# Optimization experiments

Measured on AMD Instinct MI355X. Metric: run time of the kernel, lower is better.

Reference implementation:

```python
import jax, jax.numpy as jnp
import numpy as np

B, N, M, D = 8, 4096, 4096, 3

def setup_inputs() -> dict:
    key = jax.random.key(0)
    ks = jax.random.split(key, 6)
    return {
        "X_pred": jax.random.normal(ks[0], (B, N, D), dtype=jnp.float32),
        "X_true": jax.random.normal(ks[1], (B, M, D), dtype=jnp.float32),
        "R_pred": jax.random.normal(ks[2], (B, D, D), dtype=jnp.float32),
        "t_pred": jax.random.normal(ks[3], (B, D), dtype=jnp.float32),
        "R_true": jax.random.normal(ks[4], (B, D, D), dtype=jnp.float32),
        "t_true": jax.random.normal(ks[5], (B, D), dtype=jnp.float32),
        "temperature": jnp.asarray(0.1, dtype=jnp.float32),
    }

def reference(X_pred, X_true, R_pred, t_pred, R_true, t_true, temperature):
    # Rigid transforms: x' = R x + t
    Xp = jnp.einsum('bij,bnj->bni', R_pred, X_pred) + t_pred[:, None, :]  # (B,N,D)
    Xt = jnp.einsum('bij,bmj->bmi', R_true, X_true) + t_true[:, None, :]  # (B,M,D)
    # Squared pairwise distances: |a|^2 + |b|^2 - 2 a.b  (== cdist(p=2)**2)
    sq_p = jnp.sum(Xp * Xp, axis=-1)  # (B,N)
    sq_t = jnp.sum(Xt * Xt, axis=-1)  # (B,M)
    dist_sq = sq_p[:, :, None] + sq_t[:, None, :] - 2.0 * jnp.einsum('bnd,bmd->bnm', Xp, Xt)
    dist_sq = jnp.maximum(dist_sq, 0.0)  # (B,N,M)
    soft_alignment = jax.nn.softmax(-dist_sq / temperature, axis=-1)
    weighted_distances = jnp.sum(soft_alignment * dist_sq, axis=-1)  # (B,N)
    return jnp.mean(weighted_distances)
```

## Files before the change

kernel.cpp:

```cpp
#include <hip/hip_runtime.h>


#define B_    8
#define N_    4096
#define M_    4096
#define NWAVE 8
#define BLOCK (NWAVE * 64)
#define ROWS  256
#define MSPL  8
#define QCH   (M_ / MSPL)
#define WQ    (QCH / NWAVE)
#define LOG2E 1.4426950408889634f
#define LN2   0.6931471805599453f
#define BIGF  3.0e38f

__global__ __launch_bounds__(BLOCK, 8) void softfape_main(
    const float* __restrict__ X_pred, const float* __restrict__ X_true,
    const float* __restrict__ R_pred, const float* __restrict__ t_pred,
    const float* __restrict__ R_true, const float* __restrict__ t_true,
    const float* __restrict__ temp,
    float4* __restrict__ Pg)
{
    __shared__ float4 Q[QCH];
    __shared__ float  Mp[NWAVE][ROWS];
    __shared__ float  Lp[NWAVE][ROWS];
    __shared__ float  Sp[NWAVE][ROWS];

    const int tid  = threadIdx.x;
    const int wave = tid >> 6;
    const int lane = tid & 63;
    const int x    = blockIdx.x;
    const int ms   = x & 7;
    const int rg   = (x >> 3) & 15;
    const int b    = x >> 7;

    const float T   = temp[0];
    const float c   = LOG2E / T;
    const float m2c = -2.0f * c;

    if (tid < QCH / 2) {
        const float g00 = R_true[b*9+0], g01 = R_true[b*9+1], g02 = R_true[b*9+2];
        const float g10 = R_true[b*9+3], g11 = R_true[b*9+4], g12 = R_true[b*9+5];
        const float g20 = R_true[b*9+6], g21 = R_true[b*9+7], g22 = R_true[b*9+8];
        const float u0  = t_true[b*3+0], u1 = t_true[b*3+1], u2 = t_true[b*3+2];
        const float2* xt = (const float2*)(X_true + ((size_t)b * M_ + ms * QCH) * 3);
        const float2 f0 = xt[3*tid+0], f1 = xt[3*tid+1], f2 = xt[3*tid+2];
        {
            const float y0 = fmaf(g00, f0.x, fmaf(g01, f0.y, fmaf(g02, f1.x, u0)));
            const float y1 = fmaf(g10, f0.x, fmaf(g11, f0.y, fmaf(g12, f1.x, u1)));
            const float y2 = fmaf(g20, f0.x, fmaf(g21, f0.y, fmaf(g22, f1.x, u2)));
            const float nn = fmaf(y0, y0, fmaf(y1, y1, y2 * y2));
            Q[2*tid]   = make_float4(m2c*y0, m2c*y1, m2c*y2, c*nn);
        }
        {
            const float y0 = fmaf(g00, f1.y, fmaf(g01, f2.x, fmaf(g02, f2.y, u0)));
            const float y1 = fmaf(g10, f1.y, fmaf(g11, f2.x, fmaf(g12, f2.y, u1)));
            const float y2 = fmaf(g20, f1.y, fmaf(g21, f2.x, fmaf(g22, f2.y, u2)));
            const float nn = fmaf(y0, y0, fmaf(y1, y1, y2 * y2));
            Q[2*tid+1] = make_float4(m2c*y0, m2c*y1, m2c*y2, c*nn);
        }
    }

    float px[4], py[4], pz[4], pw[4];
    {
        const float h00 = R_pred[b*9+0], h01 = R_pred[b*9+1], h02 = R_pred[b*9+2];
        const float h10 = R_pred[b*9+3], h11 = R_pred[b*9+4], h12 = R_pred[b*9+5];
        const float h20 = R_pred[b*9+6], h21 = R_pred[b*9+7], h22 = R_pred[b*9+8];
        const float v0 = t_pred[b*3+0], v1 = t_pred[b*3+1], v2 = t_pred[b*3+2];
        const float4* xp = (const float4*)(X_pred + ((size_t)b * N_ + rg * ROWS + lane * 4) * 3);
        const float4 a0 = xp[0], a1 = xp[1], a2 = xp[2];
        const float rx[4] = {a0.x, a0.w, a1.z, a2.y};
        const float ry[4] = {a0.y, a1.x, a1.w, a2.z};
        const float rz[4] = {a0.z, a1.y, a2.x, a2.w};
        #pragma unroll
        for (int r = 0; r < 4; ++r) {
            px[r] = fmaf(h00, rx[r], fmaf(h01, ry[r], fmaf(h02, rz[r], v0)));
            py[r] = fmaf(h10, rx[r], fmaf(h11, ry[r], fmaf(h12, rz[r], v1)));
            pz[r] = fmaf(h20, rx[r], fmaf(h21, ry[r], fmaf(h22, rz[r], v2)));
            pw[r] = c * fmaf(px[r], px[r], fmaf(py[r], py[r], pz[r] * pz[r]));
        }
    }

    __syncthreads();

    float mr[4] = {BIGF, BIGF, BIGF, BIGF};
    float L[4]  = {0.f, 0.f, 0.f, 0.f};
    float S[4]  = {0.f, 0.f, 0.f, 0.f};
    const float4* __restrict__ Qw = Q + wave * WQ;
    #pragma unroll 2
    for (int k = 0; k < WQ; ++k) {
        const float4 q = Qw[k];
        #pragma unroll
        for (int r = 0; r < 4; ++r) {
            const float A  = fmaf(q.x, px[r], fmaf(q.y, py[r], fmaf(q.z, pz[r], q.w)));
            const float d  = A + pw[r];
            const float mN = fminf(mr[r], d);
            const float sc = __builtin_amdgcn_exp2f(mN - mr[r]);
            const float w  = __builtin_amdgcn_exp2f(mN - d);
            L[r] = fmaf(L[r], sc, w);
            S[r] = fmaf(S[r], sc, w * d);
            mr[r] = mN;
        }
    }

    #pragma unroll
    for (int r = 0; r < 4; ++r) {
        Mp[wave][4*lane + r] = mr[r];
        Lp[wave][4*lane + r] = L[r];
        Sp[wave][4*lane + r] = S[r];
    }
    __syncthreads();

    if (tid < ROWS) {
        float m = BIGF, Lr = 0.0f, Sr = 0.0f;
        #pragma unroll
        for (int w2 = 0; w2 < NWAVE; ++w2) {
            const float mw = Mp[w2][tid];
            const float lw = Lp[w2][tid];
            const float sw = Sp[w2][tid];
            const float mN = fminf(m, mw);
            const float e1 = __builtin_amdgcn_exp2f(mN - m);
            const float e2 = __builtin_amdgcn_exp2f(mN - mw);
            Lr = Lr * e1 + lw * e2;
            Sr = Sr * e1 + sw * e2;
            m = mN;
        }
        const size_t row = (size_t)b * N_ + rg * ROWS + tid;
        Pg[row * MSPL + ms] = make_float4(m, Lr, Sr, 0.0f);
    }
}

__global__ __launch_bounds__(256) void softfape_finalize(
    const float4* __restrict__ Pg, const float* __restrict__ temp,
    float* __restrict__ out)
{
    __shared__ float ws4[4];
    const int tid = threadIdx.x;
    const size_t row = (size_t)blockIdx.x * 256 + tid;

    float m = BIGF, L = 0.0f, S = 0.0f;
    #pragma unroll
    for (int i = 0; i < MSPL; ++i) {
        const float4 P = Pg[row * MSPL + i];
        const float mN = fminf(m, P.x);
        const float e1 = __builtin_amdgcn_exp2f(mN - m);
        const float e2 = __builtin_amdgcn_exp2f(mN - P.x);
        L = L * e1 + P.y * e2;
        S = S * e1 + P.z * e2;
        m = mN;
    }
    float wd = S / L;

    wd += __shfl_xor(wd, 1);  wd += __shfl_xor(wd, 2);  wd += __shfl_xor(wd, 4);
    wd += __shfl_xor(wd, 8);  wd += __shfl_xor(wd, 16); wd += __shfl_xor(wd, 32);
    if ((tid & 63) == 0) ws4[tid >> 6] = wd;
    __syncthreads();
    if (tid == 0) {
        const float s = ws4[0] + ws4[1] + ws4[2] + ws4[3];
        const float scale = temp[0] * LN2 / ((float)B_ * (float)N_);
        atomicAdd(out, s * scale);
    }
}

extern "C" void kernel_launch(void* const* d_in, const int* in_sizes, int n_in,
                              void* d_out, int out_size, void* d_ws, size_t ws_size,
                              hipStream_t stream) {
    const float* X_pred = (const float*)d_in[0];
    const float* X_true = (const float*)d_in[1];
    const float* R_pred = (const float*)d_in[2];
    const float* t_pred = (const float*)d_in[3];
    const float* R_true = (const float*)d_in[4];
    const float* t_true = (const float*)d_in[5];
    const float* temp   = (const float*)d_in[6];
    float* out = (float*)d_out;

    float4* Pg = (float4*)d_ws;

    hipMemsetAsync(out, 0, sizeof(float), stream);

    softfape_main<<<dim3(B_ * 16 * MSPL), BLOCK, 0, stream>>>(
        X_pred, X_true, R_pred, t_pred, R_true, t_true, temp, Pg);

    softfape_finalize<<<dim3((B_ * N_) / 256), 256, 0, stream>>>(Pg, temp, out);
}
```

Measured before the change: 115.6 us.

## Replace online softmax with two-pass max-then-sum to halve exponentials

The main kernel first scans all query points to find each row's minimum scaled distance. It then makes a second pass computing a single exp per pair and accumulating sums relative to that fixed shift. This removes the per-element rescale exponential and the serial max dependency, at the cost of computing the dot product twice and adding extra block barriers. The finalize kernel is rewritten to take the global min first and then merge the partials with one exp each, and larger unrolling is applied.

```diff
diff --git a/kernel.cpp b/kernel.cpp
--- a/kernel.cpp
+++ b/kernel.cpp
@@ -25,6 +25,8 @@
     __shared__ float  Mp[NWAVE][ROWS];
     __shared__ float  Lp[NWAVE][ROWS];
     __shared__ float  Sp[NWAVE][ROWS];
+    __shared__ float  shl[ROWS];
+    __shared__ float  pwl[ROWS];
 
     const int tid  = threadIdx.x;
     const int wave = tid >> 6;
@@ -78,55 +80,66 @@
             py[r] = fmaf(h10, rx[r], fmaf(h11, ry[r], fmaf(h12, rz[r], v1)));
             pz[r] = fmaf(h20, rx[r], fmaf(h21, ry[r], fmaf(h22, rz[r], v2)));
             pw[r] = c * fmaf(px[r], px[r], fmaf(py[r], py[r], pz[r] * pz[r]));
-        }
-    }
-
-    __syncthreads();
-
-    float mr[4] = {BIGF, BIGF, BIGF, BIGF};
-    float L[4]  = {0.f, 0.f, 0.f, 0.f};
-    float S[4]  = {0.f, 0.f, 0.f, 0.f};
+            pwl[4*lane + r] = pw[r];
+        }
+    }
+
+    __syncthreads();
+
     const float4* __restrict__ Qw = Q + wave * WQ;
-    #pragma unroll 2
+
+    float mA[4] = {BIGF, BIGF, BIGF, BIGF};
+    #pragma unroll 8
     for (int k = 0; k < WQ; ++k) {
         const float4 q = Qw[k];
         #pragma unroll
         for (int r = 0; r < 4; ++r) {
-            const float A  = fmaf(q.x, px[r], fmaf(q.y, py[r], fmaf(q.z, pz[r], q.w)));
-            const float d  = A + pw[r];
-            const float mN = fminf(mr[r], d);
-            const float sc = __builtin_amdgcn_exp2f(mN - mr[r]);
-            const float w  = __builtin_amdgcn_exp2f(mN - d);
-            L[r] = fmaf(L[r], sc, w);
-            S[r] = fmaf(S[r], sc, w * d);
-            mr[r] = mN;
-        }
-    }
-
+            const float A = fmaf(q.x, px[r], fmaf(q.y, py[r], fmaf(q.z, pz[r], q.w)));
+            mA[r] = fminf(mA[r], A);
+        }
+    }
+    #pragma unroll
+    for (int r = 0; r < 4; ++r) Mp[wave][4*lane + r] = mA[r];
+    __syncthreads();
+
+    if (tid < ROWS) {
+        float m = Mp[0][tid];
+        #pragma unroll
+        for (int w2 = 1; w2 < NWAVE; ++w2) m = fminf(m, Mp[w2][tid]);
+        shl[tid] = m;
+    }
+    __syncthreads();
+
+    const float4 sh4 = *(const float4*)&shl[4*lane];
+    const float sh[4] = {sh4.x, sh4.y, sh4.z, sh4.w};
+
+    float L[4]  = {0.f, 0.f, 0.f, 0.f};
+    float SA[4] = {0.f, 0.f, 0.f, 0.f};
+    #pragma unroll 8
+    for (int k = 0; k < WQ; ++k) {
+        const float4 q = Qw[k];
+        #pragma unroll
+        for (int r = 0; r < 4; ++r) {
+            const float A   = fmaf(q.x, px[r], fmaf(q.y, py[r], fmaf(q.z, pz[r], q.w)));
+            const float arg = sh[r] - A;
+            const float w   = __builtin_amdgcn_exp2f(arg);
+            L[r] += w;
+            SA[r] = fmaf(w, arg, SA[r]);
+        }
+    }
     #pragma unroll
     for (int r = 0; r < 4; ++r) {
-        Mp[wave][4*lane + r] = mr[r];
         Lp[wave][4*lane + r] = L[r];
-        Sp[wave][4*lane + r] = S[r];
+        Sp[wave][4*lane + r] = SA[r];
     }
     __syncthreads();
 
     if (tid < ROWS) {
-        float m = BIGF, Lr = 0.0f, Sr = 0.0f;
-        #pragma unroll
-        for (int w2 = 0; w2 < NWAVE; ++w2) {
-            const float mw = Mp[w2][tid];
-            const float lw = Lp[w2][tid];
-            const float sw = Sp[w2][tid];
-            const float mN = fminf(m, mw);
-            const float e1 = __builtin_amdgcn_exp2f(mN - m);
-            const float e2 = __builtin_amdgcn_exp2f(mN - mw);
-            Lr = Lr * e1 + lw * e2;
-            Sr = Sr * e1 + sw * e2;
-            m = mN;
-        }
+        float Lr = 0.0f, Sr = 0.0f;
+        #pragma unroll
+        for (int w2 = 0; w2 < NWAVE; ++w2) { Lr += Lp[w2][tid]; Sr += Sp[w2][tid]; }
         const size_t row = (size_t)b * N_ + rg * ROWS + tid;
-        Pg[row * MSPL + ms] = make_float4(m, Lr, Sr, 0.0f);
+        Pg[row * MSPL + ms] = make_float4(shl[tid] + pwl[tid], Lr, Sr, 0.0f);
     }
 }
 
@@ -138,18 +151,23 @@
     const int tid = threadIdx.x;
     const size_t row = (size_t)blockIdx.x * 256 + tid;
 
-    float m = BIGF, L = 0.0f, S = 0.0f;
+    float4 P[MSPL];
+    #pragma unroll
+    for (int i = 0; i < MSPL; ++i) P[i] = Pg[row * MSPL + i];
+
+    float m = P[0].x;
+    #pragma unroll
+    for (int i = 1; i < MSPL; ++i) m = fminf(m, P[i].x);
+
+    float L = 0.0f, SA = 0.0f;
     #pragma unroll
     for (int i = 0; i < MSPL; ++i) {
-        const float4 P = Pg[row * MSPL + i];
-        const float mN = fminf(m, P.x);
-        const float e1 = __builtin_amdgcn_exp2f(mN - m);
-        const float e2 = __builtin_amdgcn_exp2f(mN - P.x);
-        L = L * e1 + P.y * e2;
-        S = S * e1 + P.z * e2;
-        m = mN;
-    }
-    float wd = S / L;
+        const float dm = m - P[i].x;
+        const float f  = __builtin_amdgcn_exp2f(dm);
+        L  = fmaf(P[i].y, f, L);
+        SA = fmaf(f, fmaf(dm, P[i].y, P[i].z), SA);
+    }
+    float wd = m - SA / L;
 
     wd += __shfl_xor(wd, 1);  wd += __shfl_xor(wd, 2);  wd += __shfl_xor(wd, 4);
     wd += __shfl_xor(wd, 8);  wd += __shfl_xor(wd, 16); wd += __shfl_xor(wd, 32);
```

After: 102.6 us. 11.3% less time.
